# Kernel optimization log

Measured on AMD Instinct MI355X. Metric: run time of the kernel, lower is better.

## Reference

```python
import jax, jax.numpy as jnp
import numpy as np

HEAD_DIM = 128
NUM_Q_HEAD = 16
NUM_KV_HEAD = 4
WINDOW = 1024
SOFTMAX_CAP = 30.0
SOFTMAX_TEMP = 1.0
CLIP_L, CLIP_R = -0.03, 1.03
SCALE = 1.0 / np.sqrt(HEAD_DIM).astype(np.float32)


def setup_inputs() -> dict:
    key = jax.random.key(0)
    k1, k2, k3 = jax.random.split(key, 3)
    B, S = 2, 2048
    q = jax.random.normal(k1, (B, S, NUM_Q_HEAD, HEAD_DIM), jnp.float32)
    k = jax.random.normal(k2, (B, S, NUM_KV_HEAD, HEAD_DIM), jnp.float32)
    v = jax.random.normal(k3, (B, S, NUM_KV_HEAD, HEAD_DIM), jnp.float32)
    return {"q": q, "k": k, "v": v}


def _sliding_window_attn(q, k, v):
    # q: [B,S,Hq,D]; k,v: [B,S,Hkv,D]  (BSHD layout)
    n_rep = NUM_Q_HEAD // NUM_KV_HEAD
    k = jnp.repeat(k, n_rep, axis=2)  # GQA repeat-interleave -> [B,S,Hq,D]
    v = jnp.repeat(v, n_rep, axis=2)
    # BSHD -> BHSD
    q = q.transpose(0, 2, 1, 3)
    k = k.transpose(0, 2, 1, 3)
    v = v.transpose(0, 2, 1, 3)

    P = jnp.einsum('bhqd,bhkd->bhqk', q, k)  # raw scores [B,H,S,S]

    S = q.shape[2]
    qi = jnp.arange(S)[:, None]
    kj = jnp.arange(S)[None, :]
    # causal + sliding window: allow q_idx - window <= k_idx <= q_idx
    allowed = (kj <= qi) & (kj >= qi - WINDOW)
    mask = jnp.where(allowed, 0.0, -jnp.inf).astype(P.dtype)  # [S,S]

    # softmax capping: cap * tanh(P * scale / temp) + mask
    P = SOFTMAX_CAP * jnp.tanh(P * (SCALE / SOFTMAX_TEMP)) + mask

    A = jax.nn.softmax(P, axis=-1)  # numerically stable (max-subtracted)
    # softmax clipping: clamp((r-l)*A + l, 0, 1); dropout rate is 0 -> identity
    A = jnp.clip((CLIP_R - CLIP_L) * A + CLIP_L, 0.0, 1.0)

    O = jnp.einsum('bhqk,bhkd->bhqd', A, v)
    return O.transpose(0, 2, 1, 3)  # back to BSHD


def reference(q, k, v):
    return _sliding_window_attn(q, k, v)
```

## Files before the change

### kernel.cpp

```cpp
#include <hip/hip_runtime.h>
#include <hip/hip_bf16.h>

typedef float f32x4 __attribute__((ext_vector_type(4)));
typedef _Float16 f16x8 __attribute__((ext_vector_type(8)));
typedef unsigned int u32;

#define SQ   2048
#define HQ   16
#define HKV  4
#define DH   128
#define WIN  1024
#define QT   64
#define KT   64
#define WROW 36

#define AS1 __attribute__((address_space(1)))
#define AS3 __attribute__((address_space(3)))

__device__ __forceinline__ void gload16(const void* g, void* l) {
  __builtin_amdgcn_global_load_lds((const AS1 u32*)g, (AS3 u32*)l, 16, 0, 0);
}

__device__ __forceinline__ float swa_e(float s) {
  float u = __builtin_amdgcn_exp2f(s * 0.25507046054708916f);
  return __builtin_amdgcn_exp2f(-86.5617024533378f * __builtin_amdgcn_rcpf(u + 1.0f));
}

__global__ __launch_bounds__(256)
void prep(const float* __restrict__ K, const float* __restrict__ V,
          _Float16* __restrict__ kf, _Float16* __restrict__ vt)
{
  const int t = blockIdx.x * 256 + threadIdx.x;
  const int NK = 2 * HKV * SQ * 16;
  if (t < NK) {
    const int p  = t & 15;
    const int s  = (t >> 4) & (SQ - 1);
    const int hk = (t >> 15) & 3;
    const int b  = t >> 17;
    const int c  = p ^ (s & 7);
    const float* src = K + (((size_t)b * SQ + s) * HKV + hk) * DH + c * 8;
    f32x4 x0 = *(const f32x4*)src;
    f32x4 x1 = *(const f32x4*)(src + 4);
    f16x8 o;
    #pragma unroll
    for (int j = 0; j < 4; ++j) { o[j] = (_Float16)x0[j]; o[4 + j] = (_Float16)x1[j]; }
    *(f16x8*)(kf + (((size_t)(b * HKV + hk)) * SQ + s) * DH + p * 8) = o;
  } else {
    const int u  = t - NK;
    const int p  = u & 7;
    const int d  = (u >> 3) & 127;
    const int tt = (u >> 10) & 31;
    const int hk = (u >> 15) & 3;
    const int b  = u >> 17;
    const int c  = p ^ (d & 7);
    f16x8 o;
    #pragma unroll
    for (int j = 0; j < 8; ++j) {
      const int s = tt * 64 + c * 8 + j;
      o[j] = (_Float16)V[(((size_t)b * SQ + s) * HKV + hk) * DH + d];
    }
    *(f16x8*)(vt + ((((size_t)(b * HKV + hk)) * 32 + tt) * DH + d) * 64 + p * 8) = o;
  }
}

__global__ __launch_bounds__(256, 4)
void swa_fwd(const float* __restrict__ Q, float* __restrict__ O,
             const _Float16* __restrict__ kf, const _Float16* __restrict__ vt)
{
  __shared__ _Float16 lK[KT * DH];
  __shared__ _Float16 lV[DH * KT];
  __shared__ _Float16 lW[4][16 * WROW];

  const int tid  = threadIdx.x;
  const int lane = tid & 63;
  const int wv   = tid >> 6;
  const int lm   = lane & 15;
  const int lg   = lane >> 4;

  const int bid    = blockIdx.x;
  const int stream = bid & 7;
  const int b      = stream >> 2;
  const int hk     = stream & 3;
  const int j      = bid >> 3;
  const int qt     = 31 - (j >> 2);
  const int h      = hk * 4 + (j & 3);
  const int q0     = qt * QT;

  const _Float16* kfb = kf + ((size_t)(b * HKV + hk)) * SQ * DH;
  const _Float16* vtb = vt + ((size_t)(b * HKV + hk)) * 32 * DH * 64;

  f16x8 qa[4];
  {
    const int qrow = q0 + wv * 16 + lm;
    const float* qp = Q + (((size_t)b * SQ + qrow) * HQ + h) * DH;
    #pragma unroll
    for (int kb = 0; kb < 4; ++kb) {
      const float* p = qp + kb * 32 + lg * 8;
      f32x4 x0 = *(const f32x4*)p;
      f32x4 x1 = *(const f32x4*)(p + 4);
      f16x8 a;
      #pragma unroll
      for (int jj = 0; jj < 4; ++jj) { a[jj] = (_Float16)x0[jj]; a[4 + jj] = (_Float16)x1[jj]; }
      qa[kb] = a;
    }
  }

  const int kmin = (q0 - WIN) > 0 ? (q0 - WIN) : 0;
  const int nt   = (q0 + QT - kmin) / KT;
  const int qr0  = q0 + wv * 16 + lg * 4;

  float zs[4] = {0.f, 0.f, 0.f, 0.f};
  {
    _Float16* cur = lK;
    _Float16* nxt = lV;
    {
      const char* src = (const char*)(kfb + (size_t)kmin * DH);
      #pragma unroll
      for (int r4 = 0; r4 < 4; ++r4)
        gload16(src + r4 * 4096 + wv * 1024 + lane * 16,
                (char*)cur + r4 * 4096 + wv * 1024);
    }
    __syncthreads();
    for (int t = 0; t < nt; ++t) {
      if (t + 1 < nt) {
        const char* src = (const char*)(kfb + (size_t)(kmin + (t + 1) * KT) * DH);
        #pragma unroll
        for (int r4 = 0; r4 < 4; ++r4)
          gload16(src + r4 * 4096 + wv * 1024 + lane * 16,
                  (char*)nxt + r4 * 4096 + wv * 1024);
      }
      const int  kbase = kmin + t * KT;
      const bool peel  = (t == 0 && q0 >= WIN) || (t == nt - 1);
      #pragma unroll
      for (int ks = 0; ks < 4; ++ks) {
        f32x4 acc = {0.f, 0.f, 0.f, 0.f};
        const int keyl = ks * 16 + lm;
        #pragma unroll
        for (int kb = 0; kb < 4; ++kb) {
          const int chunk = (kb * 4 + lg) ^ (keyl & 7);
          f16x8 bf = *(const f16x8*)((const char*)cur + keyl * 256 + chunk * 16);
          acc = __builtin_amdgcn_mfma_f32_16x16x32_f16(qa[kb], bf, acc, 0, 0, 0);
        }
        if (peel) {
          const int key = kbase + keyl;
          #pragma unroll
          for (int r = 0; r < 4; ++r) {
            const int qr = qr0 + r;
            const bool ok = (key <= qr) && (key >= qr - WIN);
            zs[r] += ok ? swa_e(acc[r]) : 0.f;
          }
        } else {
          #pragma unroll
          for (int r = 0; r < 4; ++r) zs[r] += swa_e(acc[r]);
        }
      }
      __syncthreads();
      _Float16* tmp = cur; cur = nxt; nxt = tmp;
    }
  }

  float rz[4], sthr[4];
  #pragma unroll
  for (int r = 0; r < 4; ++r) {
    float z = zs[r];
    z += __shfl_xor(z, 1);
    z += __shfl_xor(z, 2);
    z += __shfl_xor(z, 4);
    z += __shfl_xor(z, 8);
    rz[r] = 1.06f / z;
    float lt = __log2f(0.0283018868f * z);
    float A  = -86.5617024533378f / lt - 1.0f;
    float sv = 3.9204912f * __log2f(A) - 0.05f;
    sv = (lt >= 0.f) ? 1e30f : sv;
    sv = (lt <= -86.5617f) ? -1e30f : sv;
    sthr[r] = sv;
  }

  f32x4 oacc[8];
  #pragma unroll
  for (int i = 0; i < 8; ++i) oacc[i] = (f32x4){0.f, 0.f, 0.f, 0.f};

  for (int t = 0; t < nt; ++t) {
    const int kbase = kmin + t * KT;
    __syncthreads();
    {
      const char* kt2   = (const char*)(kfb + (size_t)kbase * DH);
      const char* vtile = (const char*)(vtb + (size_t)(kbase >> 6) * (DH * 64));
      #pragma unroll
      for (int r4 = 0; r4 < 4; ++r4) {
        gload16(kt2 + r4 * 4096 + wv * 1024 + lane * 16,
                (char*)lK + r4 * 4096 + wv * 1024);
        gload16(vtile + r4 * 4096 + wv * 1024 + lane * 16,
                (char*)lV + r4 * 4096 + wv * 1024);
      }
    }
    __syncthreads();

    const bool peel = (t == 0 && q0 >= WIN) || (t == nt - 1);

    #pragma unroll
    for (int half = 0; half < 2; ++half) {
      #pragma unroll
      for (int ks = 0; ks < 2; ++ks) {
        f32x4 acc = {0.f, 0.f, 0.f, 0.f};
        const int keyl = (half * 2 + ks) * 16 + lm;
        #pragma unroll
        for (int kb = 0; kb < 4; ++kb) {
          const int chunk = (kb * 4 + lg) ^ (keyl & 7);
          f16x8 bf = *(const f16x8*)((const char*)lK + keyl * 256 + chunk * 16);
          acc = __builtin_amdgcn_mfma_f32_16x16x32_f16(qa[kb], bf, acc, 0, 0, 0);
        }
        const int key = kbase + keyl;
        #pragma unroll
        for (int r = 0; r < 4; ++r) {
          float w = 0.f;
          if (__any(acc[r] > sthr[r])) {
            float e = swa_e(acc[r]);
            w = fminf(fmaxf(fmaf(e, rz[r], -0.03f), 0.f), 1.f);
            if (peel) {
              const int qr = qr0 + r;
              const bool ok = (key <= qr) && (key >= qr - WIN);
              w = ok ? w : 0.f;
            }
          }
          lW[wv][(lg * 4 + r) * WROW + ks * 16 + lm] = (_Float16)w;
        }
      }
      const f16x8 af = *(const f16x8*)&lW[wv][lm * WROW + lg * 8];
      #pragma unroll
      for (int dt = 0; dt < 8; ++dt) {
        const int d = dt * 16 + lm;
        const int chunk = (half * 4 + lg) ^ (d & 7);
        f16x8 bf = *(const f16x8*)((const char*)lV + d * 128 + chunk * 16);
        oacc[dt] = __builtin_amdgcn_mfma_f32_16x16x32_f16(af, bf, oacc[dt], 0, 0, 0);
      }
    }
  }

  #pragma unroll
  for (int r = 0; r < 4; ++r) {
    float* op = O + (((size_t)b * SQ + (qr0 + r)) * HQ + h) * DH;
    #pragma unroll
    for (int dt = 0; dt < 8; ++dt) op[dt * 16 + lm] = oacc[dt][r];
  }
}

extern "C" void kernel_launch(void* const* d_in, const int* in_sizes, int n_in,
                              void* d_out, int out_size, void* d_ws, size_t ws_size,
                              hipStream_t stream) {
  const float* q = (const float*)d_in[0];
  const float* k = (const float*)d_in[1];
  const float* v = (const float*)d_in[2];
  float* o = (float*)d_out;

  _Float16* kf = (_Float16*)d_ws;
  _Float16* vt = kf + (size_t)2 * HKV * SQ * DH;

  hipLaunchKernelGGL(prep, dim3(2048), dim3(256), 0, stream, k, v, kf, vt);
  hipLaunchKernelGGL(swa_fwd, dim3(1024), dim3(256), 0, stream, q, o, kf, vt);
}
```

Before: 89.59 us.

## Double query tile to 128 rows with 512-thread blocks sharing K/V tiles

Makes each block handle 128 query rows using 8 waves, so each K/V tile staged in LDS serves twice as many queries. The grid is halved and the loads are restructured so 512 threads each issue two 16-byte LDS loads per tile. The masking peel now covers the first two and last two key tiles, because the window edges span more tiles with the larger query tile. The trade is fewer blocks for load balancing and a heavier per-block register and occupancy budget under launch bounds of 512 threads with 6 blocks requested.

Result: slower. 123.6 us (+38.0%).

```diff
diff --git a/kernel.cpp b/kernel.cpp
--- a/kernel.cpp
+++ b/kernel.cpp
@@ -10,7 +10,7 @@
 #define HKV  4
 #define DH   128
 #define WIN  1024
-#define QT   64
+#define QT   128
 #define KT   64
 #define WROW 36
 
@@ -63,13 +63,13 @@
   }
 }
 
-__global__ __launch_bounds__(256, 4)
+__global__ __launch_bounds__(512, 6)
 void swa_fwd(const float* __restrict__ Q, float* __restrict__ O,
              const _Float16* __restrict__ kf, const _Float16* __restrict__ vt)
 {
   __shared__ _Float16 lK[KT * DH];
   __shared__ _Float16 lV[DH * KT];
-  __shared__ _Float16 lW[4][16 * WROW];
+  __shared__ _Float16 lW[8][16 * WROW];
 
   const int tid  = threadIdx.x;
   const int lane = tid & 63;
@@ -82,7 +82,7 @@
   const int b      = stream >> 2;
   const int hk     = stream & 3;
   const int j      = bid >> 3;
-  const int qt     = 31 - (j >> 2);
+  const int qt     = 15 - (j >> 2);
   const int h      = hk * 4 + (j & 3);
   const int q0     = qt * QT;
 
@@ -109,28 +109,23 @@
   const int nt   = (q0 + QT - kmin) / KT;
   const int qr0  = q0 + wv * 16 + lg * 4;
 
+  #define STAGE(dst, src) do {                                               \
+    gload16((const char*)(src) + wv * 1024 + lane * 16,                      \
+            (char*)(dst) + wv * 1024);                                       \
+    gload16((const char*)(src) + 8192 + wv * 1024 + lane * 16,               \
+            (char*)(dst) + 8192 + wv * 1024);                                \
+  } while (0)
+
   float zs[4] = {0.f, 0.f, 0.f, 0.f};
   {
     _Float16* cur = lK;
     _Float16* nxt = lV;
-    {
-      const char* src = (const char*)(kfb + (size_t)kmin * DH);
-      #pragma unroll
-      for (int r4 = 0; r4 < 4; ++r4)
-        gload16(src + r4 * 4096 + wv * 1024 + lane * 16,
-                (char*)cur + r4 * 4096 + wv * 1024);
-    }
+    STAGE(cur, kfb + (size_t)kmin * DH);
     __syncthreads();
     for (int t = 0; t < nt; ++t) {
-      if (t + 1 < nt) {
-        const char* src = (const char*)(kfb + (size_t)(kmin + (t + 1) * KT) * DH);
-        #pragma unroll
-        for (int r4 = 0; r4 < 4; ++r4)
-          gload16(src + r4 * 4096 + wv * 1024 + lane * 16,
-                  (char*)nxt + r4 * 4096 + wv * 1024);
-      }
+      if (t + 1 < nt) STAGE(nxt, kfb + (size_t)(kmin + (t + 1) * KT) * DH);
       const int  kbase = kmin + t * KT;
-      const bool peel  = (t == 0 && q0 >= WIN) || (t == nt - 1);
+      const bool peel  = ((q0 >= WIN) && (t <= 1)) || (t >= nt - 2);
       #pragma unroll
       for (int ks = 0; ks < 4; ++ks) {
         f32x4 acc = {0.f, 0.f, 0.f, 0.f};
@@ -183,20 +178,11 @@
   for (int t = 0; t < nt; ++t) {
     const int kbase = kmin + t * KT;
     __syncthreads();
-    {
-      const char* kt2   = (const char*)(kfb + (size_t)kbase * DH);
-      const char* vtile = (const char*)(vtb + (size_t)(kbase >> 6) * (DH * 64));
-      #pragma unroll
-      for (int r4 = 0; r4 < 4; ++r4) {
-        gload16(kt2 + r4 * 4096 + wv * 1024 + lane * 16,
-                (char*)lK + r4 * 4096 + wv * 1024);
-        gload16(vtile + r4 * 4096 + wv * 1024 + lane * 16,
-                (char*)lV + r4 * 4096 + wv * 1024);
-      }
-    }
+    STAGE(lK, kfb + (size_t)kbase * DH);
+    STAGE(lV, vtb + (size_t)(kbase >> 6) * (DH * 64));
     __syncthreads();
 
-    const bool peel = (t == 0 && q0 >= WIN) || (t == nt - 1);
+    const bool peel = ((q0 >= WIN) && (t <= 1)) || (t >= nt - 2);
 
     #pragma unroll
     for (int half = 0; half < 2; ++half) {
@@ -243,6 +229,7 @@
     #pragma unroll
     for (int dt = 0; dt < 8; ++dt) op[dt * 16 + lm] = oacc[dt][r];
   }
+  #undef STAGE
 }
 
 extern "C" void kernel_launch(void* const* d_in, const int* in_sizes, int n_in,
@@ -257,5 +244,5 @@
   _Float16* vt = kf + (size_t)2 * HKV * SQ * DH;
 
   hipLaunchKernelGGL(prep, dim3(2048), dim3(256), 0, stream, k, v, kf, vt);
-  hipLaunchKernelGGL(swa_fwd, dim3(1024), dim3(256), 0, stream, q, o, kf, vt);
-}
+  hipLaunchKernelGGL(swa_fwd, dim3(512), dim3(512), 0, stream, q, o, kf, vt);
+}
```
